# Kernel tuning notes

Measured on AMD Instinct MI355X. Metric: run time of the kernel, lower is better.

Reference implementation:

```python
import jax, jax.numpy as jnp
import numpy as np

NUM_ZONES = 256  # number of distinct zone ids per image (fill_max of zones)


def setup_inputs() -> dict:
    key = jax.random.key(0)
    k1, k2 = jax.random.split(key)
    B, H, W = 64, 512, 512
    inp = jax.random.normal(k1, (B, 1, H, W), dtype=jnp.float32)
    zones = jax.random.randint(k2, (B, H, W), 0, NUM_ZONES, dtype=jnp.int32)
    return {"input": inp, "zones": zones}


def reference(input, zones):
    # zones branch of CenterExtractor.forward: per-batch scatter_max over zone ids.
    # For each batch element, keep the pixel holding the maximum heatmap value
    # within each zone (segmented argmax), producing a boolean center mask.
    B = input.shape[0]
    x = input.reshape(B, -1)   # [B, N] flattened heatmap
    z = zones.reshape(B, -1)   # [B, N] segment ids

    # per-batch segmented max: [B, NUM_ZONES]
    seg_max = jax.vmap(
        lambda xv, zv: jax.ops.segment_max(xv, zv, num_segments=NUM_ZONES)
    )(x, z)

    # pixel is a center iff it attains its zone's max (ties measure-zero for randn;
    # empty zones have seg_max = -inf and match nothing, mirroring idxs != N filter)
    mask = x == jnp.take_along_axis(seg_max, z, axis=1)  # [B, N] bool

    centermask = mask.reshape(input.shape)  # [B, 1, H, W] bool
    n_centers = jnp.sum(centermask)
    return centermask, n_centers
```

## Files before the change

### kernel.cpp

```cpp
#include <hip/hip_runtime.h>

#define NZ    256
#define NB    64
#define NPIX  (512 * 512)

#define EPT1  32
#define CHUNK1 (256 * EPT1)
#define BPB1  (NPIX / CHUNK1)
#define NBLK1 (NB * BPB1)

#define CHUNK3 (256 * 16)
#define BPB3  (NPIX / CHUNK3)
#define NBLK3 (NB * BPB3)

__device__ __forceinline__ unsigned enc(float f) {
    unsigned b = __float_as_uint(f);
    return b ^ ((b & 0x80000000u) ? 0xFFFFFFFFu : 0x80000000u);
}
__device__ __forceinline__ float dec(unsigned u) {
    unsigned b = (u & 0x80000000u) ? (u ^ 0x80000000u) : ~u;
    return __uint_as_float(b);
}

__global__ __launch_bounds__(256) void segmax_part(
        const float* __restrict__ inp, const int* __restrict__ zones,
        unsigned* __restrict__ part) {
    __shared__ unsigned smax[NZ];
    const int t = threadIdx.x;
    smax[t] = 0u;
    __syncthreads();

    const int batch = blockIdx.x / BPB1;
    const int chunk = blockIdx.x % BPB1;
    const long base = (long)batch * NPIX + (long)chunk * CHUNK1;
    const float4* in4 = (const float4*)(inp + base);
    const int4*   z4  = (const int4*)(zones + base);

#pragma unroll
    for (int h = 0; h < EPT1 / 16; ++h) {
        float4 v[4];
        int4   z[4];
#pragma unroll
        for (int i = 0; i < 4; ++i) {
            const int idx = (h * 4 + i) * 256 + t;
            v[i] = in4[idx];
            z[i] = z4[idx];
        }
        __builtin_amdgcn_sched_barrier(0);
#pragma unroll
        for (int i = 0; i < 4; ++i) {
            atomicMax(&smax[z[i].x], enc(v[i].x));
            atomicMax(&smax[z[i].y], enc(v[i].y));
            atomicMax(&smax[z[i].z], enc(v[i].z));
            atomicMax(&smax[z[i].w], enc(v[i].w));
        }
    }
    __syncthreads();
    part[(long)blockIdx.x * NZ + t] = smax[t];
}

__global__ __launch_bounds__(256) void segmax_reduce(
        const unsigned* __restrict__ part, float* __restrict__ segf) {
    const int t = threadIdx.x;
    const int batch = blockIdx.x;
    const unsigned* p = part + (long)batch * BPB1 * NZ;
    unsigned m = 0u;
#pragma unroll 8
    for (int c = 0; c < BPB1; ++c) m = max(m, p[c * NZ + t]);
    segf[batch * NZ + t] = dec(m);
}

__global__ __launch_bounds__(256) void mask_kernel(
        const float* __restrict__ inp, const int* __restrict__ zones,
        const float* __restrict__ segf,
        int* __restrict__ mask, int* __restrict__ partial) {
    __shared__ float smax[NZ];
    __shared__ int wsum[4];
    const int t = threadIdx.x;

    const int batch = blockIdx.x / BPB3;
    const int chunk = blockIdx.x % BPB3;

    smax[t] = segf[batch * NZ + t];
    __syncthreads();

    const long base = (long)batch * NPIX + (long)chunk * CHUNK3;
    const float4* in4 = (const float4*)(inp + base);
    const int4*   z4  = (const int4*)(zones + base);
    int4* m4 = (int4*)(mask + base);

    int c = 0;
#pragma unroll
    for (int it = 0; it < 4; ++it) {
        float4 v = in4[it * 256 + t];
        int4   z = z4[it * 256 + t];
        int4 m;
        m.x = (v.x == smax[z.x]) ? 1 : 0;
        m.y = (v.y == smax[z.y]) ? 1 : 0;
        m.z = (v.z == smax[z.z]) ? 1 : 0;
        m.w = (v.w == smax[z.w]) ? 1 : 0;
        m4[it * 256 + t] = m;
        c += m.x + m.y + m.z + m.w;
    }

#pragma unroll
    for (int off = 32; off; off >>= 1) c += __shfl_down(c, off);
    if ((t & 63) == 0) wsum[t >> 6] = c;
    __syncthreads();
    if (t == 0) partial[blockIdx.x] = wsum[0] + wsum[1] + wsum[2] + wsum[3];
}

__global__ __launch_bounds__(256) void count_kernel(
        const int* __restrict__ partial, int n, int* __restrict__ count) {
    __shared__ int wsum[4];
    const int t = threadIdx.x;
    int c = 0;
    for (int i = t; i < n; i += 256) c += partial[i];
#pragma unroll
    for (int off = 32; off; off >>= 1) c += __shfl_down(c, off);
    if ((t & 63) == 0) wsum[t >> 6] = c;
    __syncthreads();
    if (t == 0) *count = wsum[0] + wsum[1] + wsum[2] + wsum[3];
}

extern "C" void kernel_launch(void* const* d_in, const int* in_sizes, int n_in,
                              void* d_out, int out_size, void* d_ws, size_t ws_size,
                              hipStream_t stream) {
    const float* inp   = (const float*)d_in[0];
    const int*   zones = (const int*)d_in[1];
    int*         out   = (int*)d_out;

    unsigned* part    = (unsigned*)d_ws;
    float*    segf    = (float*)((char*)d_ws + (size_t)NBLK1 * NZ * 4);
    int*      partial = (int*)((char*)d_ws + (size_t)NBLK1 * NZ * 4 + (size_t)NB * NZ * 4);

    const long nmask = (long)NB * NPIX;

    segmax_part  <<<NBLK1, 256, 0, stream>>>(inp, zones, part);
    segmax_reduce<<<NB,    256, 0, stream>>>(part, segf);
    mask_kernel  <<<NBLK3, 256, 0, stream>>>(inp, zones, segf, out, partial);
    count_kernel <<<1,     256, 0, stream>>>(partial, NBLK3, out + nmask);
}
```

Baseline: 56.01 us.

## Privatize shared-memory segment max into padded copies and skip redundant atomics

The first pass keeps four padded copies of the per-zone max table in shared memory, one per 16-lane group of each wavefront, so fewer lanes contend on the same address. Each pixel first does a plain LDS read and only issues atomicMax when its value exceeds the current stored max. The copies are merged before the partial results are written. This also drops the batched-load and sched_barrier structure, which can reduce memory-level parallelism, and it adds extra LDS reads per element.

```diff
diff --git a/kernel.cpp b/kernel.cpp
--- a/kernel.cpp
+++ b/kernel.cpp
@@ -9,9 +9,14 @@
 #define BPB1  (NPIX / CHUNK1)
 #define NBLK1 (NB * BPB1)
 
+#define NCPY  4
+#define NZP   264
+
 #define CHUNK3 (256 * 16)
 #define BPB3  (NPIX / CHUNK3)
 #define NBLK3 (NB * BPB3)
+
+__device__ __forceinline__ unsigned umax2(unsigned a, unsigned b) { return a > b ? a : b; }
 
 __device__ __forceinline__ unsigned enc(float f) {
     unsigned b = __float_as_uint(f);
@@ -25,10 +30,12 @@
 __global__ __launch_bounds__(256) void segmax_part(
         const float* __restrict__ inp, const int* __restrict__ zones,
         unsigned* __restrict__ part) {
-    __shared__ unsigned smax[NZ];
+    __shared__ unsigned sm[NCPY * NZP];
     const int t = threadIdx.x;
-    smax[t] = 0u;
+    for (int i = t; i < NCPY * NZP; i += 256) sm[i] = 0u;
     __syncthreads();
+
+    const int cbase = ((t & 63) >> 4) * NZP;
 
     const int batch = blockIdx.x / BPB1;
     const int chunk = blockIdx.x % BPB1;
@@ -37,26 +44,22 @@
     const int4*   z4  = (const int4*)(zones + base);
 
 #pragma unroll
-    for (int h = 0; h < EPT1 / 16; ++h) {
-        float4 v[4];
-        int4   z[4];
-#pragma unroll
-        for (int i = 0; i < 4; ++i) {
-            const int idx = (h * 4 + i) * 256 + t;
-            v[i] = in4[idx];
-            z[i] = z4[idx];
-        }
-        __builtin_amdgcn_sched_barrier(0);
-#pragma unroll
-        for (int i = 0; i < 4; ++i) {
-            atomicMax(&smax[z[i].x], enc(v[i].x));
-            atomicMax(&smax[z[i].y], enc(v[i].y));
-            atomicMax(&smax[z[i].z], enc(v[i].z));
-            atomicMax(&smax[z[i].w], enc(v[i].w));
-        }
+    for (int h = 0; h < EPT1 / 4; ++h) {
+        float4 v = in4[h * 256 + t];
+        int4   z = z4[h * 256 + t];
+        unsigned e0 = enc(v.x), e1 = enc(v.y), e2 = enc(v.z), e3 = enc(v.w);
+        const int i0 = cbase + z.x, i1 = cbase + z.y, i2 = cbase + z.z, i3 = cbase + z.w;
+        unsigned c0 = sm[i0], c1 = sm[i1], c2 = sm[i2], c3 = sm[i3];
+        if (e0 > c0) atomicMax(&sm[i0], e0);
+        if (e1 > c1) atomicMax(&sm[i1], e1);
+        if (e2 > c2) atomicMax(&sm[i2], e2);
+        if (e3 > c3) atomicMax(&sm[i3], e3);
     }
     __syncthreads();
-    part[(long)blockIdx.x * NZ + t] = smax[t];
+
+    unsigned m = umax2(umax2(sm[t], sm[NZP + t]),
+                       umax2(sm[2 * NZP + t], sm[3 * NZP + t]));
+    part[(long)blockIdx.x * NZ + t] = m;
 }
 
 __global__ __launch_bounds__(256) void segmax_reduce(
@@ -66,7 +69,7 @@
     const unsigned* p = part + (long)batch * BPB1 * NZ;
     unsigned m = 0u;
 #pragma unroll 8
-    for (int c = 0; c < BPB1; ++c) m = max(m, p[c * NZ + t]);
+    for (int c = 0; c < BPB1; ++c) m = umax2(m, p[c * NZ + t]);
     segf[batch * NZ + t] = dec(m);
 }
 
```

After: 57.51 us. 2.7% more time.

## Stage segmax loads through LDS with double-buffered async copies and skip redundant atomics

Applied to the files above, without the earlier changes.

The partial segment-max kernel now has each wave stream its quarter-chunk into a per-wave double buffer using global_load_lds, waiting on vmcnt so the next step's load overlaps the current step's atomics. Before each LDS atomicMax it reads the current zone max and skips the atomic when the value cannot raise it, cutting LDS atomic traffic. Each wave now handles one float4 per lane per step, which gives less memory-level parallelism than the earlier 4-deep register batches. The manual vmcnt accounting also depends on the compiler issuing no other vector memory operations in the loop.

```diff
diff --git a/kernel.cpp b/kernel.cpp
--- a/kernel.cpp
+++ b/kernel.cpp
@@ -4,14 +4,18 @@
 #define NB    64
 #define NPIX  (512 * 512)
 
-#define EPT1  32
-#define CHUNK1 (256 * EPT1)
-#define BPB1  (NPIX / CHUNK1)
-#define NBLK1 (NB * BPB1)
+#define EPT1    32
+#define CHUNK1  (256 * EPT1)
+#define BPB1    (NPIX / CHUNK1)
+#define NBLK1   (NB * BPB1)
+#define STEP_PX 256
+#define NSTEP   (CHUNK1 / 4 / STEP_PX)
 
 #define CHUNK3 (256 * 16)
 #define BPB3  (NPIX / CHUNK3)
 #define NBLK3 (NB * BPB3)
+
+__device__ __forceinline__ unsigned umax2(unsigned a, unsigned b) { return a > b ? a : b; }
 
 __device__ __forceinline__ unsigned enc(float f) {
     unsigned b = __float_as_uint(f);
@@ -22,38 +26,68 @@
     return __uint_as_float(b);
 }
 
+__device__ __forceinline__ void gload16(const void* g, void* l) {
+    __builtin_amdgcn_global_load_lds(
+        (const __attribute__((address_space(1))) void*)g,
+        (__attribute__((address_space(3))) void*)l, 16, 0, 0);
+}
+
 __global__ __launch_bounds__(256) void segmax_part(
         const float* __restrict__ inp, const int* __restrict__ zones,
         unsigned* __restrict__ part) {
     __shared__ unsigned smax[NZ];
+    __shared__ uint4 stage4[4][2][128];
     const int t = threadIdx.x;
+    const int lane = t & 63, wave = t >> 6;
     smax[t] = 0u;
     __syncthreads();
 
     const int batch = blockIdx.x / BPB1;
     const int chunk = blockIdx.x % BPB1;
-    const long base = (long)batch * NPIX + (long)chunk * CHUNK1;
-    const float4* in4 = (const float4*)(inp + base);
-    const int4*   z4  = (const int4*)(zones + base);
+    const long base = (long)batch * NPIX + (long)chunk * CHUNK1 + (long)wave * (CHUNK1 / 4);
+    const float* ginp = inp + base;
+    const int*   gzon = zones + base;
 
-#pragma unroll
-    for (int h = 0; h < EPT1 / 16; ++h) {
-        float4 v[4];
-        int4   z[4];
-#pragma unroll
-        for (int i = 0; i < 4; ++i) {
-            const int idx = (h * 4 + i) * 256 + t;
-            v[i] = in4[idx];
-            z[i] = z4[idx];
+    unsigned char* bufA = (unsigned char*)&stage4[wave][0][0];
+    unsigned char* bufB = (unsigned char*)&stage4[wave][1][0];
+
+    gload16(ginp + 0 * STEP_PX + 4 * lane, bufA + 16 * lane);
+    gload16(gzon + 0 * STEP_PX + 4 * lane, bufA + 1024 + 16 * lane);
+    gload16(ginp + 1 * STEP_PX + 4 * lane, bufB + 16 * lane);
+    gload16(gzon + 1 * STEP_PX + 4 * lane, bufB + 1024 + 16 * lane);
+
+    unsigned char* cur = bufA;
+    unsigned char* nxt = bufB;
+#pragma unroll 1
+    for (int s = 0; s < NSTEP - 1; ++s) {
+        asm volatile("s_waitcnt vmcnt(2)" ::: "memory");
+        __builtin_amdgcn_sched_barrier(0);
+        float4 v = ((const float4*)cur)[lane];
+        int4   z = ((const int4*)(cur + 1024))[lane];
+        unsigned e0 = enc(v.x), e1 = enc(v.y), e2 = enc(v.z), e3 = enc(v.w);
+        unsigned c0 = smax[z.x], c1 = smax[z.y], c2 = smax[z.z], c3 = smax[z.w];
+        if (e0 > c0) atomicMax(&smax[z.x], e0);
+        if (e1 > c1) atomicMax(&smax[z.y], e1);
+        if (e2 > c2) atomicMax(&smax[z.z], e2);
+        if (e3 > c3) atomicMax(&smax[z.w], e3);
+        __builtin_amdgcn_sched_barrier(0);
+        if (s + 2 < NSTEP) {
+            gload16(ginp + (s + 2) * STEP_PX + 4 * lane, cur + 16 * lane);
+            gload16(gzon + (s + 2) * STEP_PX + 4 * lane, cur + 1024 + 16 * lane);
         }
-        __builtin_amdgcn_sched_barrier(0);
-#pragma unroll
-        for (int i = 0; i < 4; ++i) {
-            atomicMax(&smax[z[i].x], enc(v[i].x));
-            atomicMax(&smax[z[i].y], enc(v[i].y));
-            atomicMax(&smax[z[i].z], enc(v[i].z));
-            atomicMax(&smax[z[i].w], enc(v[i].w));
-        }
+        unsigned char* tmp = cur; cur = nxt; nxt = tmp;
+    }
+    asm volatile("s_waitcnt vmcnt(0)" ::: "memory");
+    __builtin_amdgcn_sched_barrier(0);
+    {
+        float4 v = ((const float4*)cur)[lane];
+        int4   z = ((const int4*)(cur + 1024))[lane];
+        unsigned e0 = enc(v.x), e1 = enc(v.y), e2 = enc(v.z), e3 = enc(v.w);
+        unsigned c0 = smax[z.x], c1 = smax[z.y], c2 = smax[z.z], c3 = smax[z.w];
+        if (e0 > c0) atomicMax(&smax[z.x], e0);
+        if (e1 > c1) atomicMax(&smax[z.y], e1);
+        if (e2 > c2) atomicMax(&smax[z.z], e2);
+        if (e3 > c3) atomicMax(&smax[z.w], e3);
     }
     __syncthreads();
     part[(long)blockIdx.x * NZ + t] = smax[t];
@@ -66,7 +100,7 @@
     const unsigned* p = part + (long)batch * BPB1 * NZ;
     unsigned m = 0u;
 #pragma unroll 8
-    for (int c = 0; c < BPB1; ++c) m = max(m, p[c * NZ + t]);
+    for (int c = 0; c < BPB1; ++c) m = umax2(m, p[c * NZ + t]);
     segf[batch * NZ + t] = dec(m);
 }
 
```

After: 56.93 us. Within noise of the previous version (+1.6%).
